# Kernel tuning notes

Hardware: AMD Instinct MI355X
Metric: run time of the kernel (lower is better)

The kernel has to match this reference:

```python
import jax, jax.numpy as jnp
import numpy as np

S_MIN = 0.01
S_MAX = 36500.0
SEQ_LEN = 128
BATCH = 65536


def setup_inputs() -> dict:
    key = jax.random.key(0)
    k1, k2 = jax.random.split(key)
    # elapsed days: nonnegative floats; ratings: integers 1..4 stored as float
    t = jax.random.uniform(k1, (SEQ_LEN, BATCH), dtype=jnp.float32) * 30.0
    rating = jax.random.randint(k2, (SEQ_LEN, BATCH), 1, 5).astype(jnp.float32)
    inputs = jnp.stack([t, rating], axis=-1)  # [S, B, 2]
    w = jnp.array([0.4, 0.6, 2.4, 5.8, 4.93, 0.94, 0.86, 0.01, 1.49,
                   0.14, 0.94, 2.18, 0.05, 0.34, 1.26, 0.29, 2.61],
                  dtype=jnp.float32)
    return {"inputs": inputs, "w": w}


def _first_step(X, w):
    # state is all-zeros only on the first step (clamp keeps s >= S_MIN after)
    rating = X[:, 1]
    ridx = jnp.clip(rating.astype(jnp.int32) - 1, 0, 3)
    valid = (rating >= 1) & (rating <= 4)
    new_s = jnp.where(valid, w[ridx], 1.0)
    new_d = jnp.clip(w[4] - w[5] * (rating - 3.0), 1.0, 10.0)
    new_s = jnp.clip(new_s, S_MIN, S_MAX)
    return jnp.stack([new_s, new_d], axis=1)  # [B, 2]


def _step(w, state, X):
    s, d = state[:, 0], state[:, 1]
    t, rating = X[:, 0], X[:, 1]
    # power forgetting curve: r = (1 + t / (9 s))^-1
    r = 1.0 / (1.0 + t / (9.0 * s))
    hard_penalty = jnp.where(rating == 2, w[15], 1.0)
    easy_bonus = jnp.where(rating == 4, w[16], 1.0)
    s_success = s * (1.0 + jnp.exp(w[8]) * (11.0 - d) * jnp.power(s, -w[9])
                     * (jnp.exp((1.0 - r) * w[10]) - 1.0)
                     * hard_penalty * easy_bonus)
    s_failure = jnp.minimum(
        w[11] * jnp.power(d, -w[12]) * (jnp.power(s + 1.0, w[13]) - 1.0)
        * jnp.exp((1.0 - r) * w[14]),
        s)
    new_s = jnp.where(rating > 1.0, s_success, s_failure)
    new_d = d - w[6] * (rating - 3.0)
    new_d = w[7] * w[4] + (1.0 - w[7]) * new_d  # mean reversion to w[4]
    new_d = jnp.clip(new_d, 1.0, 10.0)
    new_s = jnp.clip(new_s, S_MIN, S_MAX)
    new_state = jnp.stack([new_s, new_d], axis=1)
    return new_state, new_state


def reference(inputs, w):
    state0 = _first_step(inputs[0], w)  # [B, 2]
    final_state, rest = jax.lax.scan(lambda st, X: _step(w, st, X),
                                     state0, inputs[1:])
    outputs = jnp.concatenate([state0[None], rest], axis=0)  # [S, B, 2]
    return outputs, final_state
```

## Files before the change

kernel.cpp:

```cpp
#include <hip/hip_runtime.h>

#define BATCH_N 65536
#define SEQ_N   128

__global__ __launch_bounds__(256) void fsrs_kernel(
    const float2* __restrict__ in,
    const float*  __restrict__ w,
    float2*       __restrict__ out)
{
    const int b = blockIdx.x * 256 + threadIdx.x;

    const float w0 = w[0], w1 = w[1], w2 = w[2], w3 = w[3];
    const float w4 = w[4], w5 = w[5], w6 = w[6], w7 = w[7];
    const float w9 = w[9], w11 = w[11], w12 = w[12], w13 = w[13];
    const float w15 = w[15], w16 = w[16];
    constexpr float LOG2E = 1.44269504088896340736f;
    const float expw8 = __builtin_amdgcn_exp2f(w[8] * LOG2E);
    const float w10l  = w[10] * LOG2E;
    const float w14l  = w[14] * LOG2E;
    const float w7w4  = w7 * w4;
    const float omw7  = 1.0f - w7;

    const float2* ip = in  + b;
    float2*       op = out + b;

    float s = 0.01f, d = 1.0f;

    auto step = [&](float2 x) {
        const float tt     = x.x;
        const float rating = x.y;
        const float nineS = 9.0f * s;
        const float r   = nineS * __builtin_amdgcn_rcpf(nineS + tt);
        const float omr = 1.0f - r;
        const float hp  = (rating == 2.0f) ? w15 : 1.0f;
        const float eb  = (rating == 4.0f) ? w16 : 1.0f;
        const float pows  = __builtin_amdgcn_exp2f(-w9 * __builtin_amdgcn_logf(s));
        const float e10   = __builtin_amdgcn_exp2f(omr * w10l);
        const float s_succ = s * (1.0f + expw8 * (11.0f - d) * pows *
                                  (e10 - 1.0f) * hp * eb);
        const float powd  = __builtin_amdgcn_exp2f(-w12 * __builtin_amdgcn_logf(d));
        const float pows1 = __builtin_amdgcn_exp2f( w13 * __builtin_amdgcn_logf(s + 1.0f));
        const float e14   = __builtin_amdgcn_exp2f(omr * w14l);
        const float s_fail = fminf(w11 * powd * (pows1 - 1.0f) * e14, s);

        const float ns = (rating > 1.0f) ? s_succ : s_fail;
        float nd = d - w6 * (rating - 3.0f);
        nd = w7w4 + omw7 * nd;
        d = fminf(fmaxf(nd, 1.0f), 10.0f);
        s = fminf(fmaxf(ns, 0.01f), 36500.0f);
    };

    float2 A[8];
#pragma unroll
    for (int i = 0; i < 8; ++i) A[i] = ip[i * BATCH_N];

    {
        float2 x = A[0];
        A[0] = ip[8 * BATCH_N];
        const float rating = x.y;
        int ri = (int)rating - 1;
        ri = ri < 0 ? 0 : (ri > 3 ? 3 : ri);
        const float wsel = (ri < 2) ? (ri == 0 ? w0 : w1)
                                    : (ri == 2 ? w2 : w3);
        const float ns = (rating >= 1.0f && rating <= 4.0f) ? wsel : 1.0f;
        const float nd = w4 - w5 * (rating - 3.0f);
        d = fminf(fmaxf(nd, 1.0f), 10.0f);
        s = fminf(fmaxf(ns, 0.01f), 36500.0f);
        op[0] = make_float2(s, d);
    }
#pragma unroll
    for (int i = 1; i < 8; ++i) {
        float2 x = A[i];
        A[i] = ip[(8 + i) * BATCH_N];
        step(x);
        op[i * BATCH_N] = make_float2(s, d);
    }

#pragma unroll 1
    for (int c = 1; c < 16; ++c) {
#pragma unroll
        for (int i = 0; i < 8; ++i) {
            float2 x = A[i];
            int tpf = c * 8 + 8 + i;
            tpf = tpf > 127 ? 127 : tpf;
            A[i] = ip[tpf * BATCH_N];
            step(x);
            op[(c * 8 + i) * BATCH_N] = make_float2(s, d);
        }
    }

    op[SEQ_N * BATCH_N] = make_float2(s, d);
}

extern "C" void kernel_launch(void* const* d_in, const int* in_sizes, int n_in,
                              void* d_out, int out_size, void* d_ws, size_t ws_size,
                              hipStream_t stream) {
    const float2* in = (const float2*)d_in[0];
    const float*  w  = (const float*)d_in[1];
    float2* out = (float2*)d_out;
    fsrs_kernel<<<BATCH_N / 256, 256, 0, stream>>>(in, w, out);
}
```

Before: 117.8 us.

## Deepen prefetch to 16 steps, use nontemporal loads/stores, and fold step arithmetic

Raises the software prefetch ring from 8 to 16 timesteps and removes the clamped prefetch index by peeling the final chunk. All global loads and stores become nontemporal, so the streaming traffic is meant to bypass cache retention. The step math is also rewritten: exp(w8) is folded into the exponent, r's complement is computed directly, the two multipliers merge into one select, and the difficulty update becomes FMAs. A deeper prefetch ring uses more registers, which may reduce occupancy.

```diff
diff --git a/kernel.cpp b/kernel.cpp
--- a/kernel.cpp
+++ b/kernel.cpp
@@ -2,11 +2,14 @@
 
 #define BATCH_N 65536
 #define SEQ_N   128
+#define DEPTH   16
+
+typedef float v2f __attribute__((ext_vector_type(2)));
 
 __global__ __launch_bounds__(256) void fsrs_kernel(
-    const float2* __restrict__ in,
-    const float*  __restrict__ w,
-    float2*       __restrict__ out)
+    const v2f* __restrict__ in,
+    const float* __restrict__ w,
+    v2f*       __restrict__ out)
 {
     const int b = blockIdx.x * 256 + threadIdx.x;
 
@@ -15,88 +18,103 @@
     const float w9 = w[9], w11 = w[11], w12 = w[12], w13 = w[13];
     const float w15 = w[15], w16 = w[16];
     constexpr float LOG2E = 1.44269504088896340736f;
-    const float expw8 = __builtin_amdgcn_exp2f(w[8] * LOG2E);
-    const float w10l  = w[10] * LOG2E;
-    const float w14l  = w[14] * LOG2E;
-    const float w7w4  = w7 * w4;
-    const float omw7  = 1.0f - w7;
+    const float w8l  = w[8]  * LOG2E;
+    const float w10l = w[10] * LOG2E;
+    const float w14l = w[14] * LOG2E;
+    const float omw7   = 1.0f - w7;
+    const float omw7w6 = omw7 * w6;
+    const float dc0    = w7 * w4 + 3.0f * omw7w6;
 
-    const float2* ip = in  + b;
-    float2*       op = out + b;
+    const v2f* ip = in  + b;
+    v2f*       op = out + b;
 
     float s = 0.01f, d = 1.0f;
 
-    auto step = [&](float2 x) {
+    auto step = [&](v2f x) {
         const float tt     = x.x;
         const float rating = x.y;
         const float nineS = 9.0f * s;
-        const float r   = nineS * __builtin_amdgcn_rcpf(nineS + tt);
-        const float omr = 1.0f - r;
-        const float hp  = (rating == 2.0f) ? w15 : 1.0f;
-        const float eb  = (rating == 4.0f) ? w16 : 1.0f;
-        const float pows  = __builtin_amdgcn_exp2f(-w9 * __builtin_amdgcn_logf(s));
+        const float rc  = __builtin_amdgcn_rcpf(nineS + tt);
+        const float omr = tt * rc;
+        const float hb = (rating == 2.0f) ? w15 : ((rating == 4.0f) ? w16 : 1.0f);
+
+        const float log2s = __builtin_amdgcn_logf(s);
+        const float ex    = __builtin_amdgcn_exp2f(__builtin_fmaf(-w9, log2s, w8l));
         const float e10   = __builtin_amdgcn_exp2f(omr * w10l);
-        const float s_succ = s * (1.0f + expw8 * (11.0f - d) * pows *
-                                  (e10 - 1.0f) * hp * eb);
-        const float powd  = __builtin_amdgcn_exp2f(-w12 * __builtin_amdgcn_logf(d));
-        const float pows1 = __builtin_amdgcn_exp2f( w13 * __builtin_amdgcn_logf(s + 1.0f));
-        const float e14   = __builtin_amdgcn_exp2f(omr * w14l);
+        const float su    = ex * (11.0f - d) * (e10 - 1.0f) * hb;
+        const float s_succ = __builtin_fmaf(su, s, s);
+
+        const float log2d  = __builtin_amdgcn_logf(d);
+        const float powd   = __builtin_amdgcn_exp2f(-w12 * log2d);
+        const float log2s1 = __builtin_amdgcn_logf(s + 1.0f);
+        const float pows1  = __builtin_amdgcn_exp2f(w13 * log2s1);
+        const float e14    = __builtin_amdgcn_exp2f(omr * w14l);
         const float s_fail = fminf(w11 * powd * (pows1 - 1.0f) * e14, s);
 
         const float ns = (rating > 1.0f) ? s_succ : s_fail;
-        float nd = d - w6 * (rating - 3.0f);
-        nd = w7w4 + omw7 * nd;
+        const float nd = __builtin_fmaf(omw7, d, __builtin_fmaf(-omw7w6, rating, dc0));
         d = fminf(fmaxf(nd, 1.0f), 10.0f);
         s = fminf(fmaxf(ns, 0.01f), 36500.0f);
     };
 
-    float2 A[8];
+    auto st = [&](int idx) {
+        v2f o; o.x = s; o.y = d;
+        __builtin_nontemporal_store(o, &op[idx]);
+    };
+
+    v2f A[DEPTH];
 #pragma unroll
-    for (int i = 0; i < 8; ++i) A[i] = ip[i * BATCH_N];
+    for (int i = 0; i < DEPTH; ++i)
+        A[i] = __builtin_nontemporal_load(&ip[i * BATCH_N]);
 
     {
-        float2 x = A[0];
-        A[0] = ip[8 * BATCH_N];
+        v2f x = A[0];
+        A[0] = __builtin_nontemporal_load(&ip[DEPTH * BATCH_N]);
         const float rating = x.y;
-        int ri = (int)rating - 1;
-        ri = ri < 0 ? 0 : (ri > 3 ? 3 : ri);
-        const float wsel = (ri < 2) ? (ri == 0 ? w0 : w1)
-                                    : (ri == 2 ? w2 : w3);
+        const float wsel = (rating < 2.5f) ? ((rating < 1.5f) ? w0 : w1)
+                                           : ((rating < 3.5f) ? w2 : w3);
         const float ns = (rating >= 1.0f && rating <= 4.0f) ? wsel : 1.0f;
         const float nd = w4 - w5 * (rating - 3.0f);
         d = fminf(fmaxf(nd, 1.0f), 10.0f);
         s = fminf(fmaxf(ns, 0.01f), 36500.0f);
-        op[0] = make_float2(s, d);
+        st(0);
     }
 #pragma unroll
-    for (int i = 1; i < 8; ++i) {
-        float2 x = A[i];
-        A[i] = ip[(8 + i) * BATCH_N];
+    for (int i = 1; i < DEPTH; ++i) {
+        v2f x = A[i];
+        A[i] = __builtin_nontemporal_load(&ip[(DEPTH + i) * BATCH_N]);
         step(x);
-        op[i * BATCH_N] = make_float2(s, d);
+        st(i * BATCH_N);
     }
 
 #pragma unroll 1
-    for (int c = 1; c < 16; ++c) {
+    for (int c = 1; c < 7; ++c) {
 #pragma unroll
-        for (int i = 0; i < 8; ++i) {
-            float2 x = A[i];
-            int tpf = c * 8 + 8 + i;
-            tpf = tpf > 127 ? 127 : tpf;
-            A[i] = ip[tpf * BATCH_N];
+        for (int i = 0; i < DEPTH; ++i) {
+            v2f x = A[i];
+            A[i] = __builtin_nontemporal_load(&ip[((c + 1) * DEPTH + i) * BATCH_N]);
             step(x);
-            op[(c * 8 + i) * BATCH_N] = make_float2(s, d);
+            st((c * DEPTH + i) * BATCH_N);
         }
     }
 
-    op[SEQ_N * BATCH_N] = make_float2(s, d);
+#pragma unroll
+    for (int i = 0; i < DEPTH; ++i) {
+        step(A[i]);
+        st((7 * DEPTH + i) * BATCH_N);
+    }
+
+    {
+        v2f o; o.x = s; o.y = d;
+        op[SEQ_N * BATCH_N] = o;
+    }
 }
 
 extern "C" void kernel_launch(void* const* d_in, const int* in_sizes, int n_in,
                               void* d_out, int out_size, void* d_ws, size_t ws_size,
                               hipStream_t stream) {
-    const float2* in = (const float2*)d_in[0];
-    const float*  w  = (const float*)d_in[1];
-    float2* out = (float2*)d_out;
+    const v2f*   in = (const v2f*)d_in[0];
+    const float* w  = (const float*)d_in[1];
+    v2f* out = (v2f*)d_out;
     fsrs_kernel<<<BATCH_N / 256, 256, 0, stream>>>(in, w, out);
 }
```

After: 119.3 us. Within noise of the previous version (+1.3%).
